# Kernel tuning notes

Measured on AMD Instinct MI355X. Metric: run time of the kernel, lower is better.

## Reference

```python
import jax, jax.numpy as jnp
import numpy as np

N = 50000
IN_C = 256
HID = 64
C = 4
HC = HID * C  # 256
OUT_C = 64
E = 800000
L = 2
BETA = 0.1
TEMP = 1.0
EPS = 1e-5


def layer_norm(x, g, b):
    mu = jnp.mean(x, axis=-1, keepdims=True)
    var = jnp.mean((x - mu) ** 2, axis=-1, keepdims=True)
    return (x - mu) * jax.lax.rsqrt(var + EPS) * g + b


def setup_inputs() -> dict:
    key = jax.random.key(0)
    ks = jax.random.split(key, 12)
    x = jax.random.normal(ks[0], (N, IN_C), dtype=jnp.float32)
    # edges without self-loops (remove_self_loops is then a no-op)
    row = jax.random.randint(ks[1], (E,), 0, N)
    off = jax.random.randint(ks[2], (E,), 1, N)
    col = (row + off) % N
    edge_index = jnp.stack([row, col]).astype(jnp.int64)
    s_in = 1.0 / np.sqrt(IN_C)
    s_hc = 1.0 / np.sqrt(HC)
    s_h = 1.0 / np.sqrt(HID)
    W1 = jax.random.uniform(ks[3], (IN_C, HC), minval=-s_in, maxval=s_in)
    b1 = jax.random.uniform(ks[4], (HC,), minval=-s_in, maxval=s_in)
    lin_ws = jax.random.uniform(ks[5], (L, HC, HID), minval=-s_hc, maxval=s_hc)
    att_ws = jax.random.uniform(ks[6], (L, HID, C), minval=-s_h, maxval=s_h)
    ln_gs = jnp.ones((L + 1, HC), dtype=jnp.float32)
    ln_bs = jnp.zeros((L + 1, HC), dtype=jnp.float32)
    W2 = jax.random.uniform(ks[7], (HC, OUT_C), minval=-s_hc, maxval=s_hc)
    b2 = jax.random.uniform(ks[8], (OUT_C,), minval=-s_hc, maxval=s_hc)
    return dict(x=x, edge_index=edge_index, W1=W1, b1=b1, lin_ws=lin_ws,
                att_ws=att_ws, ln_gs=ln_gs, ln_bs=ln_bs, W2=W2, b2=b2)


def reference(x, edge_index, W1, b1, lin_ws, att_ws, ln_gs, ln_bs, W2, b2):
    row, col = edge_index[0], edge_index[1]
    x = jax.nn.relu(x @ W1 + b1)              # [N, HC]
    x = layer_norm(x, ln_gs[0], ln_bs[0])
    ego = x
    for i in range(L):
        h = x @ lin_ws[i]                      # [N, HID]
        h_col = h[col]                         # [E, HID]
        br = jax.nn.relu(0.5 * h[row] + h_col) @ att_ws[i]   # [E, C]
        a = jax.nn.softmax(br / TEMP, axis=1)  # [E, C]
        # concat c gated copies: [a0*h_col, a1*h_col, ...] -> [E, C*HID]
        x_j = (a[:, :, None] * h_col[:, None, :]).reshape(E, C * HID)
        out = jax.ops.segment_sum(x_j, row, num_segments=N)   # [N, HC]
        x = jax.nn.relu(out)
        x = layer_norm(x, ln_gs[i + 1], ln_bs[i + 1])
        x = (1.0 - BETA) * x + BETA * ego
    logits = x @ W2 + b2
    return jax.nn.log_softmax(logits, axis=1)
```

## Files before the change

### kernel.cpp

```cpp
#include <hip/hip_runtime.h>
#include <cstdint>

static constexpr float kEps  = 1e-5f;
static constexpr float kBeta = 0.1f;
static constexpr int   kCap  = 128;

typedef __attribute__((ext_vector_type(8))) short bf16x8;
typedef __attribute__((ext_vector_type(4))) float f32x4;

__device__ __forceinline__ ushort f2bf(float f){
  uint u = __float_as_uint(f);
  u += 0x7fff + ((u>>16)&1);
  return (ushort)(u>>16);
}
__device__ __forceinline__ float bf2f(ushort h){
  return __uint_as_float(((uint)h)<<16);
}

__global__ void k_hist_bin(const int* __restrict__ row, int* __restrict__ deg,
                           int E, int NR){
  const int p  = blockIdx.x & 7;
  const int q  = blockIdx.x >> 3;
  const int NQ = gridDim.x >> 3;
  const int lo = p*NR, hi = lo + NR;
  for (int e = q*256 + threadIdx.x; e < E; e += NQ*256){
    int r = row[e];
    if (r >= lo && r < hi) atomicAdd(&deg[r], 1);
  }
}

__global__ void k_scan_block(const int* __restrict__ deg, int* __restrict__ start,
                             int* __restrict__ bsum, int N){
  __shared__ int s[256];
  int t = threadIdx.x;
  int i = blockIdx.x*256 + t;
  int v = (i < N) ? deg[i] : 0;
  s[t] = v; __syncthreads();
  for (int off=1; off<256; off<<=1){
    int add = (t >= off) ? s[t-off] : 0;
    __syncthreads();
    s[t] += add;
    __syncthreads();
  }
  if (i < N) start[i+1] = s[t];
  if (t == 255) bsum[blockIdx.x] = s[255];
}

__global__ void k_scan_bsum(const int* __restrict__ bsum, int* __restrict__ boff, int nb){
  __shared__ int s[256];
  int t = threadIdx.x;
  int v = (t < nb) ? bsum[t] : 0;
  s[t] = v; __syncthreads();
  for (int off=1; off<256; off<<=1){
    int add = (t >= off) ? s[t-off] : 0;
    __syncthreads();
    s[t] += add;
    __syncthreads();
  }
  if (t < nb) boff[t] = s[t] - v;
}

__global__ void k_scan_add(int* __restrict__ start, const int* __restrict__ boff, int N){
  int i = blockIdx.x*256 + threadIdx.x;
  if (i < N) start[i+1] += boff[blockIdx.x];
  if (blockIdx.x==0 && threadIdx.x==0) start[0] = 0;
}

__global__ void k_fill_bin(const int* __restrict__ row, const int* __restrict__ col,
                           const int* __restrict__ start, int* __restrict__ cursor,
                           int* __restrict__ colcsr, int E, int NR){
  const int p  = blockIdx.x & 7;
  const int q  = blockIdx.x >> 3;
  const int NQ = gridDim.x >> 3;
  const int lo = p*NR, hi = lo + NR;
  for (int e = q*256 + threadIdx.x; e < E; e += NQ*256){
    int r = row[e];
    if (r >= lo && r < hi){
      int pos = atomicAdd(&cursor[r], 1);
      colcsr[start[r] + pos] = col[e];
    }
  }
}

__global__ void k_rowfill(const int* __restrict__ start, int* __restrict__ rowcsr, int N){
  int n = blockIdx.x*256 + threadIdx.x;
  if (n < N){
    int s0 = start[n], s1 = start[n+1];
    for (int i=s0; i<s1; ++i) rowcsr[i] = n;
  }
}

__global__ void k_prep_w1(const float* __restrict__ W1, ushort* __restrict__ W1s){
  int i = blockIdx.x*256 + threadIdx.x;
  int k = i >> 8, col = i & 255;
  W1s[(k>>5)*8192 + col*32 + (k&31)] = f2bf(W1[i]);
}

__global__ void k_prep_w64(const float* __restrict__ W,
                           ushort* __restrict__ Wh, ushort* __restrict__ Wl){
  int i = blockIdx.x*256 + threadIdx.x;
  int k = i >> 6, col = i & 63;
  int dst = (k>>5)*2048 + col*32 + (k&31);
  float w = W[i];
  ushort hb = f2bf(w);
  Wh[dst] = hb;
  Wl[dst] = f2bf(w - bf2f(hb));
}

__global__ __launch_bounds__(256) void k_gemm1_mfma(const float* __restrict__ x,
    const ushort* __restrict__ W1s, const float* __restrict__ b1,
    const float* __restrict__ g, const float* __restrict__ bb,
    ushort* __restrict__ ego, int N){
  __shared__ ushort xh[64][40];
  __shared__ ushort xl[64][40];
  __shared__ ushort wl[256][40];
  __shared__ float psum[64][4], psq[64][4];
  __shared__ float mub[64], ivb[64];

  const int tid = threadIdx.x;
  const int n0  = blockIdx.x*64;
  const int w   = tid>>6;
  const int l   = tid&63;
  const int l15 = l&15;
  const int lg  = l>>4;
  const int cb  = w*64;
  const int sxr = tid>>2;
  const int sxk = (tid&3)*8;

  f32x4 acc[4][4];
  #pragma unroll
  for (int rt=0;rt<4;rt++)
    #pragma unroll
    for (int ct=0;ct<4;ct++)
      acc[rt][ct] = (f32x4){0.f,0.f,0.f,0.f};

  for (int kc=0; kc<8; ++kc){
    if (kc) __syncthreads();
    const float* xp = &x[(size_t)min(n0+sxr, N-1)*256 + kc*32 + sxk];
    float4 v0 = *reinterpret_cast<const float4*>(xp);
    float4 v1 = *reinterpret_cast<const float4*>(xp+4);
    const float vv[8] = {v0.x,v0.y,v0.z,v0.w,v1.x,v1.y,v1.z,v1.w};
    bf16x8 hv, lv;
    #pragma unroll
    for (int j=0;j<8;j++){
      ushort hb = f2bf(vv[j]);
      hv[j] = (short)hb;
      lv[j] = (short)f2bf(vv[j] - bf2f(hb));
    }
    *reinterpret_cast<bf16x8*>(&xh[sxr][sxk]) = hv;
    *reinterpret_cast<bf16x8*>(&xl[sxr][sxk]) = lv;
    #pragma unroll
    for (int s2=0;s2<4;s2++){
      int rowi = (tid>>2) + s2*64;
      *reinterpret_cast<bf16x8*>(&wl[rowi][(tid&3)*8]) =
          *reinterpret_cast<const bf16x8*>(&W1s[kc*8192 + rowi*32 + (tid&3)*8]);
    }
    __syncthreads();
    bf16x8 ah[4], al[4];
    #pragma unroll
    for (int rt=0;rt<4;rt++){
      ah[rt] = *reinterpret_cast<const bf16x8*>(&xh[rt*16+l15][lg*8]);
      al[rt] = *reinterpret_cast<const bf16x8*>(&xl[rt*16+l15][lg*8]);
    }
    #pragma unroll
    for (int ct=0;ct<4;ct++){
      bf16x8 bv = *reinterpret_cast<const bf16x8*>(&wl[cb+ct*16+l15][lg*8]);
      #pragma unroll
      for (int rt=0;rt<4;rt++){
        acc[rt][ct] = __builtin_amdgcn_mfma_f32_16x16x32_bf16(al[rt], bv, acc[rt][ct], 0,0,0);
        acc[rt][ct] = __builtin_amdgcn_mfma_f32_16x16x32_bf16(ah[rt], bv, acc[rt][ct], 0,0,0);
      }
    }
  }

  float b1v[4], gv[4], bbv[4];
  #pragma unroll
  for (int ct=0;ct<4;ct++){
    int col = cb + ct*16 + l15;
    b1v[ct] = b1[col]; gv[ct] = g[col]; bbv[ct] = bb[col];
  }
  #pragma unroll
  for (int rt=0;rt<4;rt++)
    #pragma unroll
    for (int ct=0;ct<4;ct++)
      #pragma unroll
      for (int r=0;r<4;r++)
        acc[rt][ct][r] = fmaxf(acc[rt][ct][r] + b1v[ct], 0.f);

  #pragma unroll
  for (int rt=0;rt<4;rt++){
    #pragma unroll
    for (int r=0;r<4;r++){
      float s = acc[rt][0][r]+acc[rt][1][r]+acc[rt][2][r]+acc[rt][3][r];
      float q = acc[rt][0][r]*acc[rt][0][r]+acc[rt][1][r]*acc[rt][1][r]
              + acc[rt][2][r]*acc[rt][2][r]+acc[rt][3][r]*acc[rt][3][r];
      #pragma unroll
      for (int o=1;o<16;o<<=1){ s += __shfl_xor(s,o); q += __shfl_xor(q,o); }
      if (l15 == 0){
        int row = rt*16 + lg*4 + r;
        psum[row][w] = s; psq[row][w] = q;
      }
    }
  }
  __syncthreads();
  if (tid < 64){
    float s = psum[tid][0]+psum[tid][1]+psum[tid][2]+psum[tid][3];
    float q = psq[tid][0]+psq[tid][1]+psq[tid][2]+psq[tid][3];
    float mu  = s * (1.f/256.f);
    float var = q * (1.f/256.f) - mu*mu;
    mub[tid] = mu;
    ivb[tid] = rsqrtf(fmaxf(var, 0.f) + kEps);
  }
  __syncthreads();
  #pragma unroll
  for (int rt=0;rt<4;rt++){
    #pragma unroll
    for (int r=0;r<4;r++){
      int row  = rt*16 + lg*4 + r;
      int grow = n0 + row;
      if (grow < N){
        float mu = mub[row], inv = ivb[row];
        size_t base = (size_t)grow*256 + cb + l15;
        #pragma unroll
        for (int ct=0;ct<4;ct++)
          ego[base + ct*16] = f2bf((acc[rt][ct][r]-mu)*inv*gv[ct] + bbv[ct]);
      }
    }
  }
}

__global__ __launch_bounds__(256) void k_hgemm_mfma(const ushort* __restrict__ x,
    const ushort* __restrict__ Wh, const ushort* __restrict__ Wl,
    ushort* __restrict__ h, int N){
  __shared__ ushort xs[64][40];
  __shared__ ushort wh[64][40];
  __shared__ ushort wl[64][40];
  const int tid = threadIdx.x;
  const int n0  = blockIdx.x*64;
  const int w   = tid>>6;
  const int l15 = tid&15;
  const int lg  = (tid&63)>>4;
  const int sxr = tid>>2;
  const int sxk = (tid&3)*8;

  f32x4 acc[4];
  #pragma unroll
  for (int ct=0;ct<4;ct++) acc[ct] = (f32x4){0.f,0.f,0.f,0.f};

  for (int kc=0; kc<8; ++kc){
    if (kc) __syncthreads();
    *reinterpret_cast<bf16x8*>(&xs[sxr][sxk]) =
        *reinterpret_cast<const bf16x8*>(&x[(size_t)min(n0+sxr, N-1)*256 + kc*32 + sxk]);
    int src = kc*2048 + sxr*32 + sxk;
    *reinterpret_cast<bf16x8*>(&wh[sxr][sxk]) =
        *reinterpret_cast<const bf16x8*>(&Wh[src]);
    *reinterpret_cast<bf16x8*>(&wl[sxr][sxk]) =
        *reinterpret_cast<const bf16x8*>(&Wl[src]);
    __syncthreads();
    bf16x8 ah = *reinterpret_cast<const bf16x8*>(&xs[w*16+l15][lg*8]);
    #pragma unroll
    for (int ct=0;ct<4;ct++){
      bf16x8 bh = *reinterpret_cast<const bf16x8*>(&wh[ct*16+l15][lg*8]);
      bf16x8 bl = *reinterpret_cast<const bf16x8*>(&wl[ct*16+l15][lg*8]);
      acc[ct] = __builtin_amdgcn_mfma_f32_16x16x32_bf16(ah, bl, acc[ct], 0,0,0);
      acc[ct] = __builtin_amdgcn_mfma_f32_16x16x32_bf16(ah, bh, acc[ct], 0,0,0);
    }
  }
  #pragma unroll
  for (int r=0;r<4;r++){
    int grow = n0 + w*16 + lg*4 + r;
    if (grow < N){
      #pragma unroll
      for (int ct=0;ct<4;ct++)
        h[(size_t)grow*64 + ct*16 + l15] = f2bf(acc[ct][r]);
    }
  }
}

__global__ __launch_bounds__(256) void k_out_mfma(const ushort* __restrict__ x,
    const ushort* __restrict__ Wh, const ushort* __restrict__ Wl,
    const float* __restrict__ b2, float* __restrict__ out, int N){
  __shared__ ushort xs[64][40];
  __shared__ ushort wh[64][40];
  __shared__ ushort wl[64][40];
  const int tid = threadIdx.x;
  const int n0  = blockIdx.x*64;
  const int w   = tid>>6;
  const int l15 = tid&15;
  const int lg  = (tid&63)>>4;
  const int sxr = tid>>2;
  const int sxk = (tid&3)*8;

  f32x4 acc[4];
  #pragma unroll
  for (int ct=0;ct<4;ct++) acc[ct] = (f32x4){0.f,0.f,0.f,0.f};

  for (int kc=0; kc<8; ++kc){
    if (kc) __syncthreads();
    *reinterpret_cast<bf16x8*>(&xs[sxr][sxk]) =
        *reinterpret_cast<const bf16x8*>(&x[(size_t)min(n0+sxr, N-1)*256 + kc*32 + sxk]);
    int src = kc*2048 + sxr*32 + sxk;
    *reinterpret_cast<bf16x8*>(&wh[sxr][sxk]) =
        *reinterpret_cast<const bf16x8*>(&Wh[src]);
    *reinterpret_cast<bf16x8*>(&wl[sxr][sxk]) =
        *reinterpret_cast<const bf16x8*>(&Wl[src]);
    __syncthreads();
    bf16x8 ah = *reinterpret_cast<const bf16x8*>(&xs[w*16+l15][lg*8]);
    #pragma unroll
    for (int ct=0;ct<4;ct++){
      bf16x8 bh = *reinterpret_cast<const bf16x8*>(&wh[ct*16+l15][lg*8]);
      bf16x8 bl = *reinterpret_cast<const bf16x8*>(&wl[ct*16+l15][lg*8]);
      acc[ct] = __builtin_amdgcn_mfma_f32_16x16x32_bf16(ah, bl, acc[ct], 0,0,0);
      acc[ct] = __builtin_amdgcn_mfma_f32_16x16x32_bf16(ah, bh, acc[ct], 0,0,0);
    }
  }

  float b2v[4];
  #pragma unroll
  for (int ct=0;ct<4;ct++) b2v[ct] = b2[ct*16+l15];

  #pragma unroll
  for (int r=0;r<4;r++){
    float v[4];
    #pragma unroll
    for (int ct=0;ct<4;ct++) v[ct] = acc[ct][r] + b2v[ct];
    float mx = fmaxf(fmaxf(v[0],v[1]), fmaxf(v[2],v[3]));
    #pragma unroll
    for (int o=1;o<16;o<<=1) mx = fmaxf(mx, __shfl_xor(mx,o));
    float sm = __expf(v[0]-mx)+__expf(v[1]-mx)+__expf(v[2]-mx)+__expf(v[3]-mx);
    #pragma unroll
    for (int o=1;o<16;o<<=1) sm += __shfl_xor(sm,o);
    float ls = __logf(sm);
    int grow = n0 + w*16 + lg*4 + r;
    if (grow < N){
      #pragma unroll
      for (int ct=0;ct<4;ct++)
        out[(size_t)grow*64 + ct*16 + l15] = (v[ct]-mx) - ls;
    }
  }
}

__global__ __launch_bounds__(256) void k_att_agg(
    const ushort* __restrict__ h,
    const int* __restrict__ rowcsr, const int* __restrict__ colcsr,
    const int* __restrict__ start,
    const float* __restrict__ attw,
    const ushort* __restrict__ ego,
    const float* __restrict__ g, const float* __restrict__ b,
    ushort* __restrict__ xout, int N){
  __shared__ ushort s_hc[kCap][72];
  __shared__ float4 s_a[kCap];

  const int tid  = threadIdx.x;
  const int lane = tid & 63;
  const int wid  = tid >> 6;
  const int grp  = lane >> 4;
  const int l15  = lane & 15;
  const int nb   = blockIdx.x*4;
  const int n    = nb + wid;

  const int b0 = start[nb];
  const int b1 = start[min(nb+4, N)];
  const int s0 = (n < N) ? start[n]   : b1;
  const int s1 = (n < N) ? start[n+1] : b1;
  const size_t hoff = (size_t)l15*4;

  float acc[4][4];
  #pragma unroll
  for (int c=0;c<4;c++)
    #pragma unroll
    for (int j=0;j<4;j++) acc[c][j]=0.f;

  for (int base = b0; base < b1; base += kCap){
    const int cnt = min(b1 - base, kCap);
    for (int e = tid; e < cnt; e += 256){
      int edge = base + e;
      int r = rowcsr[edge], c = colcsr[edge];
      const uint4* hrp = reinterpret_cast<const uint4*>(h + (size_t)r*64);
      const uint4* hcp = reinterpret_cast<const uint4*>(h + (size_t)c*64);
      float q0=0.f, q1=0.f, q2=0.f, q3=0.f;
      #pragma unroll
      for (int s=0; s<8; ++s){
        uint4 hr4 = hrp[s];
        uint4 hc4 = hcp[s];
        *reinterpret_cast<uint4*>(&s_hc[e][s*8]) = hc4;
        const uint hru[4] = {hr4.x, hr4.y, hr4.z, hr4.w};
        const uint hcu[4] = {hc4.x, hc4.y, hc4.z, hc4.w};
        #pragma unroll
        for (int t=0; t<4; ++t){
          float hrl = __uint_as_float(hru[t]<<16);
          float hrh = __uint_as_float(hru[t]&0xffff0000u);
          float hcl = __uint_as_float(hcu[t]<<16);
          float hch = __uint_as_float(hcu[t]&0xffff0000u);
          float pl = fmaxf(fmaf(0.5f, hrl, hcl), 0.f);
          float ph = fmaxf(fmaf(0.5f, hrh, hch), 0.f);
          int d = s*8 + t*2;
          float4 w0 = *reinterpret_cast<const float4*>(&attw[(d  )*4]);
          float4 w1 = *reinterpret_cast<const float4*>(&attw[(d+1)*4]);
          q0 = fmaf(pl, w0.x, q0); q1 = fmaf(pl, w0.y, q1);
          q2 = fmaf(pl, w0.z, q2); q3 = fmaf(pl, w0.w, q3);
          q0 = fmaf(ph, w1.x, q0); q1 = fmaf(ph, w1.y, q1);
          q2 = fmaf(ph, w1.z, q2); q3 = fmaf(ph, w1.w, q3);
        }
      }
      float m = fmaxf(fmaxf(q0,q1), fmaxf(q2,q3));
      float e0=__expf(q0-m), e1=__expf(q1-m), e2=__expf(q2-m), e3=__expf(q3-m);
      float inv = 1.f/(e0+e1+e2+e3);
      s_a[e] = make_float4(e0*inv, e1*inv, e2*inv, e3*inv);
    }
    __syncthreads();
    int lo = max(s0, base), hi = min(s1, base + cnt);
    for (int i = lo + grp; i < hi; i += 4){
      int e = i - base;
      float4 av = s_a[e];
      ushort4 hv = *reinterpret_cast<const ushort4*>(&s_hc[e][l15*4]);
      float d0=bf2f(hv.x), d1=bf2f(hv.y), d2=bf2f(hv.z), d3=bf2f(hv.w);
      acc[0][0]=fmaf(av.x,d0,acc[0][0]); acc[0][1]=fmaf(av.x,d1,acc[0][1]);
      acc[0][2]=fmaf(av.x,d2,acc[0][2]); acc[0][3]=fmaf(av.x,d3,acc[0][3]);
      acc[1][0]=fmaf(av.y,d0,acc[1][0]); acc[1][1]=fmaf(av.y,d1,acc[1][1]);
      acc[1][2]=fmaf(av.y,d2,acc[1][2]); acc[1][3]=fmaf(av.y,d3,acc[1][3]);
      acc[2][0]=fmaf(av.z,d0,acc[2][0]); acc[2][1]=fmaf(av.z,d1,acc[2][1]);
      acc[2][2]=fmaf(av.z,d2,acc[2][2]); acc[2][3]=fmaf(av.z,d3,acc[2][3]);
      acc[3][0]=fmaf(av.w,d0,acc[3][0]); acc[3][1]=fmaf(av.w,d1,acc[3][1]);
      acc[3][2]=fmaf(av.w,d2,acc[3][2]); acc[3][3]=fmaf(av.w,d3,acc[3][3]);
    }
    __syncthreads();
  }

  if (n >= N) return;

  #pragma unroll
  for (int c=0;c<4;c++)
    #pragma unroll
    for (int j=0;j<4;j++){
      float v = acc[c][j];
      v += __shfl_xor(v,16);
      v += __shfl_xor(v,32);
      acc[c][j] = fmaxf(v, 0.f);
    }

  float s=0.f, sq=0.f;
  #pragma unroll
  for (int c=0;c<4;c++)
    #pragma unroll
    for (int j=0;j<4;j++){ float v=acc[c][j]; s+=v; sq+=v*v; }
  #pragma unroll
  for (int o=1;o<16;o<<=1){ s += __shfl_xor(s,o); sq += __shfl_xor(sq,o); }
  float mu  = s * (1.f/256.f);
  float var = sq * (1.f/256.f) - mu*mu;
  float inv = rsqrtf(fmaxf(var,0.f) + kEps);

  int colb = grp*64 + l15*4;
  float4 gv  = *reinterpret_cast<const float4*>(&g[colb]);
  float4 bv  = *reinterpret_cast<const float4*>(&b[colb]);
  size_t base2 = (size_t)n*256 + colb;
  ushort4 ev = *reinterpret_cast<const ushort4*>(&ego[base2]);
  ushort4 y;
  y.x = f2bf((1.f-kBeta)*((acc[grp][0]-mu)*inv*gv.x + bv.x) + kBeta*bf2f(ev.x));
  y.y = f2bf((1.f-kBeta)*((acc[grp][1]-mu)*inv*gv.y + bv.y) + kBeta*bf2f(ev.y));
  y.z = f2bf((1.f-kBeta)*((acc[grp][2]-mu)*inv*gv.z + bv.z) + kBeta*bf2f(ev.z));
  y.w = f2bf((1.f-kBeta)*((acc[grp][3]-mu)*inv*gv.w + bv.w) + kBeta*bf2f(ev.w));
  *reinterpret_cast<ushort4*>(&xout[base2]) = y;
}

extern "C" void kernel_launch(void* const* d_in, const int* in_sizes, int n_in,
                              void* d_out, int out_size, void* d_ws, size_t ws_size,
                              hipStream_t stream){
  const float* x_in = (const float*)d_in[0];
  const int*   ei   = (const int*)d_in[1];
  const float* W1   = (const float*)d_in[2];
  const float* b1   = (const float*)d_in[3];
  const float* lin  = (const float*)d_in[4];
  const float* att  = (const float*)d_in[5];
  const float* lng  = (const float*)d_in[6];
  const float* lnb  = (const float*)d_in[7];
  const float* W2   = (const float*)d_in[8];
  const float* b2   = (const float*)d_in[9];
  float* out = (float*)d_out;

  const int N = in_sizes[0] / 256;
  const int E = in_sizes[1] / 2;
  const int* row = ei;
  const int* col = ei + E;

  char* basep = (char*)d_ws;
  size_t off = 0;
  auto alloc = [&](size_t bytes)->char*{
    char* p = basep + off;
    off += (bytes + 255) & ~(size_t)255;
    return p;
  };
  ushort* ego    = (ushort*)alloc((size_t)N*256*2);
  ushort* xbuf   = (ushort*)alloc((size_t)N*256*2);
  ushort* hbuf   = (ushort*)alloc((size_t)N*64*2);
  int*    startp = (int*)   alloc((size_t)(N+1)*4);
  int*    deg    = (int*)   alloc((size_t)N*4);
  int*    rowcsr = (int*)   alloc((size_t)E*4);
  int*    colcsr = (int*)   alloc((size_t)E*4);
  int*    bsum   = (int*)   alloc(256*4);
  int*    boff   = (int*)   alloc(256*4);
  ushort* W1s    = (ushort*)alloc((size_t)256*256*2);
  ushort* linh   = (ushort*)alloc((size_t)2*16384*2);
  ushort* linl   = (ushort*)alloc((size_t)2*16384*2);
  ushort* W2h    = (ushort*)alloc((size_t)16384*2);
  ushort* W2l    = (ushort*)alloc((size_t)16384*2);

  int nbN = (N + 255)/256;
  int nbT = (N + 63)/64;
  int NR  = (N + 7)/8;

  hipMemsetAsync(deg, 0, (size_t)N*4, stream);
  k_hist_bin<<<1024,256,0,stream>>>(row, deg, E, NR);
  k_scan_block<<<nbN,256,0,stream>>>(deg, startp, bsum, N);
  k_scan_bsum<<<1,256,0,stream>>>(bsum, boff, nbN);
  k_scan_add<<<nbN,256,0,stream>>>(startp, boff, N);
  hipMemsetAsync(deg, 0, (size_t)N*4, stream);
  k_fill_bin<<<1024,256,0,stream>>>(row, col, startp, deg, colcsr, E, NR);
  k_rowfill<<<nbN,256,0,stream>>>(startp, rowcsr, N);

  k_prep_w1<<<256,256,0,stream>>>(W1, W1s);
  k_prep_w64<<<64,256,0,stream>>>(lin,          linh,          linl);
  k_prep_w64<<<64,256,0,stream>>>(lin + 16384,  linh + 16384,  linl + 16384);
  k_prep_w64<<<64,256,0,stream>>>(W2, W2h, W2l);

  k_gemm1_mfma<<<nbT,256,0,stream>>>(x_in, W1s, b1, lng, lnb, ego, N);

  for (int L=0; L<2; ++L){
    const ushort* xsrc = (L == 0) ? ego : xbuf;
    k_hgemm_mfma<<<nbT,256,0,stream>>>(xsrc, linh + (size_t)L*16384,
                                       linl + (size_t)L*16384, hbuf, N);
    k_att_agg<<<(N+3)/4,256,0,stream>>>(hbuf, rowcsr, colcsr, startp,
                                        att + (size_t)L*64*4, ego,
                                        lng + (size_t)(L+1)*256, lnb + (size_t)(L+1)*256,
                                        xbuf, N);
  }
  k_out_mfma<<<nbT,256,0,stream>>>(xbuf, W2h, W2l, b2, out, N);
}
```

Before: 292.7 us.

## Shrink attention-aggregate block to one wavefront handling four nodes

The attention aggregation kernel now runs 64-thread blocks. Each 16-lane group owns one node and accumulates all four channel copies itself, where before a 256-thread block used one wavefront per node and split edges across groups. This removes the cross-group shuffle reduction, shrinks shared memory, and cuts barrier cost in a block that is a single wavefront. The trade-off is that each group walks its node's edges serially and there are fewer threads per block to hide gather latency, which could hurt high-degree nodes.

```diff
diff --git a/kernel.cpp b/kernel.cpp
--- a/kernel.cpp
+++ b/kernel.cpp
@@ -3,7 +3,6 @@
 
 static constexpr float kEps  = 1e-5f;
 static constexpr float kBeta = 0.1f;
-static constexpr int   kCap  = 128;
 
 typedef __attribute__((ext_vector_type(8))) short bf16x8;
 typedef __attribute__((ext_vector_type(4))) float f32x4;
@@ -340,7 +339,7 @@
   }
 }
 
-__global__ __launch_bounds__(256) void k_att_agg(
+__global__ __launch_bounds__(64) void k_att_agg(
     const ushort* __restrict__ h,
     const int* __restrict__ rowcsr, const int* __restrict__ colcsr,
     const int* __restrict__ start,
@@ -348,22 +347,19 @@
     const ushort* __restrict__ ego,
     const float* __restrict__ g, const float* __restrict__ b,
     ushort* __restrict__ xout, int N){
-  __shared__ ushort s_hc[kCap][72];
-  __shared__ float4 s_a[kCap];
-
-  const int tid  = threadIdx.x;
-  const int lane = tid & 63;
-  const int wid  = tid >> 6;
+  __shared__ ushort s_hc[64][72];
+  __shared__ float4 s_a[64];
+
+  const int lane = threadIdx.x;
   const int grp  = lane >> 4;
   const int l15  = lane & 15;
   const int nb   = blockIdx.x*4;
-  const int n    = nb + wid;
+  const int n    = nb + grp;
 
   const int b0 = start[nb];
   const int b1 = start[min(nb+4, N)];
   const int s0 = (n < N) ? start[n]   : b1;
   const int s1 = (n < N) ? start[n+1] : b1;
-  const size_t hoff = (size_t)l15*4;
 
   float acc[4][4];
   #pragma unroll
@@ -371,10 +367,10 @@
     #pragma unroll
     for (int j=0;j<4;j++) acc[c][j]=0.f;
 
-  for (int base = b0; base < b1; base += kCap){
-    const int cnt = min(b1 - base, kCap);
-    for (int e = tid; e < cnt; e += 256){
-      int edge = base + e;
+  for (int base = b0; base < b1; base += 64){
+    const int cnt = min(b1 - base, 64);
+    if (lane < cnt){
+      int edge = base + lane;
       int r = rowcsr[edge], c = colcsr[edge];
       const uint4* hrp = reinterpret_cast<const uint4*>(h + (size_t)r*64);
       const uint4* hcp = reinterpret_cast<const uint4*>(h + (size_t)c*64);
@@ -383,7 +379,7 @@
       for (int s=0; s<8; ++s){
         uint4 hr4 = hrp[s];
         uint4 hc4 = hcp[s];
-        *reinterpret_cast<uint4*>(&s_hc[e][s*8]) = hc4;
+        *reinterpret_cast<uint4*>(&s_hc[lane][s*8]) = hc4;
         const uint hru[4] = {hr4.x, hr4.y, hr4.z, hr4.w};
         const uint hcu[4] = {hc4.x, hc4.y, hc4.z, hc4.w};
         #pragma unroll
@@ -406,11 +402,11 @@
       float m = fmaxf(fmaxf(q0,q1), fmaxf(q2,q3));
       float e0=__expf(q0-m), e1=__expf(q1-m), e2=__expf(q2-m), e3=__expf(q3-m);
       float inv = 1.f/(e0+e1+e2+e3);
-      s_a[e] = make_float4(e0*inv, e1*inv, e2*inv, e3*inv);
+      s_a[lane] = make_float4(e0*inv, e1*inv, e2*inv, e3*inv);
     }
     __syncthreads();
     int lo = max(s0, base), hi = min(s1, base + cnt);
-    for (int i = lo + grp; i < hi; i += 4){
+    for (int i = lo; i < hi; ++i){
       int e = i - base;
       float4 av = s_a[e];
       ushort4 hv = *reinterpret_cast<const ushort4*>(&s_hc[e][l15*4]);
@@ -424,7 +420,7 @@
       acc[3][0]=fmaf(av.w,d0,acc[3][0]); acc[3][1]=fmaf(av.w,d1,acc[3][1]);
       acc[3][2]=fmaf(av.w,d2,acc[3][2]); acc[3][3]=fmaf(av.w,d3,acc[3][3]);
     }
-    __syncthreads();
+    if (base + 64 < b1) __syncthreads();
   }
 
   if (n >= N) return;
@@ -432,12 +428,8 @@
   #pragma unroll
   for (int c=0;c<4;c++)
     #pragma unroll
-    for (int j=0;j<4;j++){
-      float v = acc[c][j];
-      v += __shfl_xor(v,16);
-      v += __shfl_xor(v,32);
-      acc[c][j] = fmaxf(v, 0.f);
-    }
+    for (int j=0;j<4;j++)
+      acc[c][j] = fmaxf(acc[c][j], 0.f);
 
   float s=0.f, sq=0.f;
   #pragma unroll
@@ -450,17 +442,20 @@
   float var = sq * (1.f/256.f) - mu*mu;
   float inv = rsqrtf(fmaxf(var,0.f) + kEps);
 
-  int colb = grp*64 + l15*4;
-  float4 gv  = *reinterpret_cast<const float4*>(&g[colb]);
-  float4 bv  = *reinterpret_cast<const float4*>(&b[colb]);
-  size_t base2 = (size_t)n*256 + colb;
-  ushort4 ev = *reinterpret_cast<const ushort4*>(&ego[base2]);
-  ushort4 y;
-  y.x = f2bf((1.f-kBeta)*((acc[grp][0]-mu)*inv*gv.x + bv.x) + kBeta*bf2f(ev.x));
-  y.y = f2bf((1.f-kBeta)*((acc[grp][1]-mu)*inv*gv.y + bv.y) + kBeta*bf2f(ev.y));
-  y.z = f2bf((1.f-kBeta)*((acc[grp][2]-mu)*inv*gv.z + bv.z) + kBeta*bf2f(ev.z));
-  y.w = f2bf((1.f-kBeta)*((acc[grp][3]-mu)*inv*gv.w + bv.w) + kBeta*bf2f(ev.w));
-  *reinterpret_cast<ushort4*>(&xout[base2]) = y;
+  size_t nbase = (size_t)n*256;
+  #pragma unroll
+  for (int c=0;c<4;c++){
+    int colb = c*64 + l15*4;
+    float4 gv  = *reinterpret_cast<const float4*>(&g[colb]);
+    float4 bv  = *reinterpret_cast<const float4*>(&b[colb]);
+    ushort4 ev = *reinterpret_cast<const ushort4*>(&ego[nbase + colb]);
+    ushort4 y;
+    y.x = f2bf((1.f-kBeta)*((acc[c][0]-mu)*inv*gv.x + bv.x) + kBeta*bf2f(ev.x));
+    y.y = f2bf((1.f-kBeta)*((acc[c][1]-mu)*inv*gv.y + bv.y) + kBeta*bf2f(ev.y));
+    y.z = f2bf((1.f-kBeta)*((acc[c][2]-mu)*inv*gv.z + bv.z) + kBeta*bf2f(ev.z));
+    y.w = f2bf((1.f-kBeta)*((acc[c][3]-mu)*inv*gv.w + bv.w) + kBeta*bf2f(ev.w));
+    *reinterpret_cast<ushort4*>(&xout[nbase + colb]) = y;
+  }
 }
 
 extern "C" void kernel_launch(void* const* d_in, const int* in_sizes, int n_in,
@@ -529,10 +524,10 @@
     const ushort* xsrc = (L == 0) ? ego : xbuf;
     k_hgemm_mfma<<<nbT,256,0,stream>>>(xsrc, linh + (size_t)L*16384,
                                        linl + (size_t)L*16384, hbuf, N);
-    k_att_agg<<<(N+3)/4,256,0,stream>>>(hbuf, rowcsr, colcsr, startp,
-                                        att + (size_t)L*64*4, ego,
-                                        lng + (size_t)(L+1)*256, lnb + (size_t)(L+1)*256,
-                                        xbuf, N);
+    k_att_agg<<<(N+3)/4,64,0,stream>>>(hbuf, rowcsr, colcsr, startp,
+                                       att + (size_t)L*64*4, ego,
+                                       lng + (size_t)(L+1)*256, lnb + (size_t)(L+1)*256,
+                                       xbuf, N);
   }
   k_out_mfma<<<nbT,256,0,stream>>>(xbuf, W2h, W2l, b2, out, N);
 }
```

Result: faster. 253.6 us (-13.4%).
